# Optimization experiments

Hardware: AMD Instinct MI355X
Metric: run time of the kernel (lower is better)

## Reference

```python
import jax, jax.numpy as jnp
import numpy as np

N, E, IN = 50000, 800000, 128   # nodes, edges, input feature dim
H, C = 8, 32                    # heads, per-head channels
HC = H * C                      # 256 = concat width
NEG_SLOPE = 0.2
BN_EPS = 1e-5


def _gat_conv(x, src, dst, W, a_src, a_dst, b, heads, out_ch, concat):
    """PyG-style GATConv (eval mode, self-loops already in src/dst)."""
    n = x.shape[0]
    h = (x @ W).reshape(n, heads, out_ch)                 # [N,H,C]
    alpha_s = (h * a_src).sum(-1)                         # [N,H]
    alpha_d = (h * a_dst).sum(-1)                         # [N,H]
    e = jax.nn.leaky_relu(alpha_s[src] + alpha_d[dst], NEG_SLOPE)  # [Etot,H]
    # segment softmax over destination nodes (every node has a self-loop)
    emax = jax.ops.segment_max(e, dst, num_segments=n)    # [N,H]
    e = jnp.exp(e - emax[dst])
    denom = jax.ops.segment_sum(e, dst, num_segments=n)
    alpha = e / (denom[dst] + 1e-16)                      # [Etot,H]
    msg = h[src] * alpha[:, :, None]                      # [Etot,H,C]
    out = jax.ops.segment_sum(msg, dst, num_segments=n)   # [N,H,C]
    out = out.reshape(n, heads * out_ch) if concat else out.mean(axis=1)
    return out + b


def _bn(y, g, beta, m, v):
    return (y - m) * jax.lax.rsqrt(v + BN_EPS) * g + beta


def setup_inputs() -> dict:
    key = jax.random.key(0)
    ks = jax.random.split(key, 32)
    def p(i, shape, s=0.1):
        return jax.random.normal(ks[i], shape, dtype=jnp.float32) * s
    x = jax.random.normal(ks[0], (N, IN), dtype=jnp.float32)
    edge_index = jax.random.randint(ks[1], (2, E), 0, N, dtype=jnp.int32)
    d = dict(
        x=x, edge_index=edge_index,
        W1=p(2, (IN, HC)), a_src1=p(3, (H, C)), a_dst1=p(4, (H, C)), b1=p(5, (HC,)),
        bn1_g=jnp.ones((HC,), jnp.float32), bn1_b=jnp.zeros((HC,), jnp.float32),
        bn1_m=p(6, (HC,)), bn1_v=jax.random.uniform(ks[7], (HC,), jnp.float32, 0.5, 1.5),
        W2=p(8, (HC, HC)), a_src2=p(9, (H, C)), a_dst2=p(10, (H, C)), b2=p(11, (HC,)),
        bn2_g=jnp.ones((HC,), jnp.float32), bn2_b=jnp.zeros((HC,), jnp.float32),
        bn2_m=p(12, (HC,)), bn2_v=jax.random.uniform(ks[13], (HC,), jnp.float32, 0.5, 1.5),
        W3=p(14, (HC, C)), a_src3=p(15, (1, C)), a_dst3=p(16, (1, C)), b3=p(17, (C,)),
        Ws1=p(18, (IN, HC)), bs1=p(19, (HC,)),
        Ws2=p(20, (HC, C)), bs2=p(21, (C,)),
    )
    return d


def reference(x, edge_index, W1, a_src1, a_dst1, b1, bn1_g, bn1_b, bn1_m, bn1_v,
              W2, a_src2, a_dst2, b2, bn2_g, bn2_b, bn2_m, bn2_v,
              W3, a_src3, a_dst3, b3, Ws1, bs1, Ws2, bs2):
    n = x.shape[0]
    loops = jnp.arange(n, dtype=edge_index.dtype)
    src = jnp.concatenate([edge_index[0], loops])   # PyG add_self_loops=True
    dst = jnp.concatenate([edge_index[1], loops])
    x0 = x @ Ws1 + bs1                               # skip1
    h = _gat_conv(x, src, dst, W1, a_src1, a_dst1, b1, H, C, True)
    h = jax.nn.elu(_bn(h, bn1_g, bn1_b, bn1_m, bn1_v)) + x0
    xs = h @ Ws2 + bs2                               # skip2
    h2 = _gat_conv(h, src, dst, W2, a_src2, a_dst2, b2, H, C, True)
    h2 = jax.nn.elu(_bn(h2, bn2_g, bn2_b, bn2_m, bn2_v))
    out = _gat_conv(h2, src, dst, W3, a_src3, a_dst3, b3, 1, C, False) + xs
    return out
```

## Files before the change

### kernel.cpp

```cpp
#include <hip/hip_runtime.h>
#include <hip/hip_bf16.h>

#define NEG_SLOPE 0.2f
#define BN_EPS 1e-5f
#define BSH 8
#define STASH_CAP 6400

typedef __attribute__((ext_vector_type(8))) short bf16x8;
typedef __attribute__((ext_vector_type(4))) float f32x4;
typedef __attribute__((ext_vector_type(2))) float f32x2;

#if defined(__has_builtin)
#if __has_builtin(__builtin_amdgcn_cvt_f32_fp8) && __has_builtin(__builtin_amdgcn_cvt_pk_fp8_f32)
#define HW_FP8 1
#endif
#if __has_builtin(__builtin_amdgcn_cvt_pk_f32_fp8)
#define HW_FP8_PK 1
#endif
#endif

__device__ __forceinline__ float bf2f(unsigned short u) {
    union { unsigned int i; float f; } x;
    x.i = ((unsigned int)u) << 16;
    return x.f;
}
__device__ __forceinline__ unsigned short f2bf(float f) {
    __hip_bfloat16 b = __float2bfloat16(f);
    return *reinterpret_cast<unsigned short*>(&b);
}
__device__ __forceinline__ float lrelu(float v) {
    return v > 0.f ? v : NEG_SLOPE * v;
}
__device__ __forceinline__ void gload_lds16(const void* g, void* l) {
    __builtin_amdgcn_global_load_lds(
        (const __attribute__((address_space(1))) unsigned int*)(g),
        (__attribute__((address_space(3))) unsigned int*)(l),
        16, 0, 0);
}

__device__ __forceinline__ unsigned char f8enc(float f) {
#ifdef HW_FP8
    int p = __builtin_amdgcn_cvt_pk_fp8_f32(f, 0.f, 0, false);
    return (unsigned char)(p & 0xff);
#else
    float a = fabsf(f);
    unsigned int sign = (__float_as_uint(f) >> 31) << 7;
    if (a < 0.0009765625f) return (unsigned char)sign;
    a = fminf(a, 448.f);
    unsigned int bits = __float_as_uint(a);
    int e = (int)((bits >> 23) & 0xff) - 127;
    unsigned int mant = bits & 0x7fffff;
    if (e < -6) {
        int q = (int)(a * 512.f + 0.5f);
        if (q >= 8) return (unsigned char)(sign | 0x08);
        return (unsigned char)(sign | q);
    }
    unsigned int m = mant >> 20;
    unsigned int rem = mant & 0xfffff;
    if (rem > 0x80000 || (rem == 0x80000 && (m & 1))) m++;
    if (m == 8) { m = 0; e++; }
    if (e > 8) { e = 8; m = 6; }
    return (unsigned char)(sign | ((unsigned int)(e + 7) << 3) | m);
#endif
}
template <int SEL>
__device__ __forceinline__ float f8dec(unsigned int w) {
#ifdef HW_FP8
    return __builtin_amdgcn_cvt_f32_fp8(w, SEL);
#else
    unsigned int b = (w >> (SEL * 8)) & 0xff;
    unsigned int s = b >> 7, em = b & 0x7f;
    float mag;
    if (em >= 8) {
        unsigned int bits = (((em >> 3) + 120) << 23) | ((em & 7) << 20);
        mag = __uint_as_float(bits);
    } else {
        mag = (float)em * 0.001953125f;
    }
    return s ? -mag : mag;
#endif
}
__device__ __forceinline__ void fma_f8x4(float we, unsigned int wv, float4& acc) {
#ifdef HW_FP8_PK
    f32x2 lo = __builtin_amdgcn_cvt_pk_f32_fp8((int)wv, false);
    f32x2 hi = __builtin_amdgcn_cvt_pk_f32_fp8((int)wv, true);
    acc.x = fmaf(we, lo[0], acc.x);
    acc.y = fmaf(we, lo[1], acc.y);
    acc.z = fmaf(we, hi[0], acc.z);
    acc.w = fmaf(we, hi[1], acc.w);
#else
    acc.x = fmaf(we, f8dec<0>(wv), acc.x);
    acc.y = fmaf(we, f8dec<1>(wv), acc.y);
    acc.z = fmaf(we, f8dec<2>(wv), acc.z);
    acc.w = fmaf(we, f8dec<3>(wv), acc.w);
#endif
}

__device__ __forceinline__ int block_scan_incl(int v, int t) {
    int lane = t & 63, w = t >> 6;
    int sv = v;
    #pragma unroll
    for (int off = 1; off < 64; off <<= 1) {
        int u = __shfl_up(sv, off);
        if (lane >= off) sv += u;
    }
    __shared__ int ws_[4];
    if (lane == 63) ws_[w] = sv;
    __syncthreads();
    if (t == 0) {
        int a = 0;
        #pragma unroll
        for (int k = 0; k < 4; k++) { int x = ws_[k]; ws_[k] = a; a += x; }
    }
    __syncthreads();
    return sv + ws_[w];
}

__global__ __launch_bounds__(256) void phase1(const int* __restrict__ dstl,
                                              int E, int N, int NB,
                                              int* __restrict__ gHist,
                                              const float* __restrict__ x,
                                              unsigned short* __restrict__ xb, int n4x,
                                              const float* __restrict__ W1,
                                              const float* __restrict__ Ws1,
                                              const float* __restrict__ W2,
                                              const float* __restrict__ Ws2,
                                              const float* __restrict__ W3,
                                              const float* __restrict__ a_src1,
                                              const float* __restrict__ a_dst1,
                                              const float* __restrict__ a_src2,
                                              const float* __restrict__ a_dst2,
                                              const float* __restrict__ a_src3,
                                              const float* __restrict__ a_dst3,
                                              unsigned short* __restrict__ Wcat1,
                                              unsigned short* __restrict__ Wcat2,
                                              unsigned short* __restrict__ W3t) {
    int t = threadIdx.x;
    if (blockIdx.x < 256) {
        __shared__ int h[256];
        h[t] = 0;
        __syncthreads();
        int Etot = E + N;
        for (int i = blockIdx.x * 256 + t; i < Etot; i += 256 * 256) {
            int d = (i < E) ? dstl[i] : (i - E);
            atomicAdd(&h[d >> BSH], 1);
        }
        __syncthreads();
        if (t < NB && h[t]) atomicAdd(&gHist[t], h[t]);
        return;
    }
    int i = (blockIdx.x - 256) * 256 + t;
    if (i < n4x) {
        float4 v = reinterpret_cast<const float4*>(x)[i];
        ushort4 o;
        o.x = f2bf(v.x); o.y = f2bf(v.y); o.z = f2bf(v.z); o.w = f2bf(v.w);
        reinterpret_cast<ushort4*>(xb)[i] = o;
        return;
    }
    int j = i - n4x;
    if (j < 32768) {
        int m = j >> 7, k = j & 127;
        Wcat1[j] = f2bf(W1[k * 256 + m]);
    } else if (j < 65536) {
        int q = j - 32768; int m = q >> 7, k = q & 127;
        Wcat1[32768 + q] = f2bf(Ws1[k * 256 + m]);
    } else if (j < 131072) {
        int q = j - 65536; int m = q >> 8, k = q & 255;
        Wcat2[q] = f2bf(W2[k * 256 + m]);
    } else if (j < 139264) {
        int q = j - 131072; int m = q >> 8, k = q & 255;
        Wcat2[65536 + q] = f2bf(Ws2[k * 32 + m]);
    } else if (j < 147456) {
        int q = j - 139264; int m = q >> 8, k = q & 255;
        W3t[q] = f2bf(W3[k * 32 + m]);
    } else if (j < 149504) {
        int q = j - 147456; int r = q >> 7, k = q & 127;
        int h = r & 7;
        const float* av = (r < 8) ? a_src1 : a_dst1;
        float s = 0.f;
        #pragma unroll
        for (int c = 0; c < 32; c++) s += W1[k * 256 + h * 32 + c] * av[h * 32 + c];
        Wcat1[(512 + r) * 128 + k] = f2bf(s);
    } else if (j < 153600) {
        int q = j - 149504; int r = q >> 8, k = q & 255;
        int h = r & 7;
        const float* av = (r < 8) ? a_src2 : a_dst2;
        float s = 0.f;
        #pragma unroll
        for (int c = 0; c < 32; c++) s += W2[k * 256 + h * 32 + c] * av[h * 32 + c];
        Wcat2[(288 + r) * 256 + k] = f2bf(s);
    } else if (j < 154112) {
        int q = j - 153600; int r = q >> 8, k = q & 255;
        const float* av = r ? a_dst3 : a_src3;
        float s = 0.f;
        #pragma unroll
        for (int c = 0; c < 32; c++) s += W3[k * 32 + c] * av[c];
        W3t[(32 + r) * 256 + k] = f2bf(s);
    }
}

__global__ __launch_bounds__(256) void bucket_scatter(const int* __restrict__ srcl,
                                                      const int* __restrict__ dstl,
                                                      int E, int N, int NB,
                                                      const int* __restrict__ gHist,
                                                      int* __restrict__ gCursor,
                                                      unsigned int* __restrict__ bktEdges) {
    __shared__ unsigned int stage[4096];
    __shared__ int lbase[256];
    __shared__ int hist[256];
    __shared__ int bexcl[257];
    __shared__ int curk[256];
    __shared__ int gbase[256];
    int t = threadIdx.x;
    int Etot = E + N;
    int begin = blockIdx.x * 4096;

    int gv = (t < NB) ? gHist[t] : 0;
    int gincl = block_scan_incl(gv, t);
    lbase[t] = gincl - gv;
    __syncthreads();

    hist[t] = 0;
    __syncthreads();

    unsigned int ent[16];
    int eb[16];
    #pragma unroll
    for (int k = 0; k < 16; k++) {
        int i = begin + k * 256 + t;
        if (i < Etot) {
            int s, d;
            if (i < E) { s = srcl[i]; d = dstl[i]; }
            else       { s = d = i - E; }
            eb[k] = d >> BSH;
            ent[k] = ((unsigned int)s << BSH) | (unsigned int)(d & 255);
            atomicAdd(&hist[eb[k]], 1);
        } else eb[k] = -1;
    }
    __syncthreads();

    int v = hist[t];
    int incl = block_scan_incl(v, t);
    bexcl[t] = incl - v;
    curk[t] = incl - v;
    if (t == 255) bexcl[256] = incl;
    __syncthreads();

    #pragma unroll
    for (int k = 0; k < 16; k++) {
        if (eb[k] >= 0) {
            int slot = atomicAdd(&curk[eb[k]], 1);
            stage[slot] = ent[k];
        }
    }
    if (t < NB) {
        int cnt = hist[t];
        gbase[t] = cnt ? (lbase[t] + atomicAdd(&gCursor[t], cnt)) : 0;
    }
    __syncthreads();

    int total = bexcl[256];
    for (int p = t; p < total; p += 256) {
        int lo = 0, hi = NB - 1;
        while (lo < hi) {
            int mid = (lo + hi + 1) >> 1;
            if (bexcl[mid] <= p) lo = mid; else hi = mid - 1;
        }
        bktEdges[gbase[lo] + (p - bexcl[lo])] = stage[p];
    }
}

__global__ __launch_bounds__(256) void bucket_to_csr(const unsigned int* __restrict__ bktEdges,
                                                     const int* __restrict__ gHist,
                                                     int* __restrict__ indptr,
                                                     int* __restrict__ esrc,
                                                     int N, int NB, int Etot) {
    __shared__ int lbase[256];
    __shared__ int nh[256];
    __shared__ int ncur[256];
    __shared__ unsigned int stash[STASH_CAP];
    int b = blockIdx.x, t = threadIdx.x;

    int gv = (t < NB) ? gHist[t] : 0;
    int gincl = block_scan_incl(gv, t);
    lbase[t] = gincl - gv;
    __syncthreads();
    int base = lbase[b];
    int cnt = gHist[b];
    int nodeBase = b << BSH;

    nh[t] = 0;
    __syncthreads();
    for (int p = t; p < cnt; p += 256) {
        unsigned int e = bktEdges[base + p];
        if (p < STASH_CAP) stash[p] = e;
        atomicAdd(&nh[e & 255], 1);
    }
    __syncthreads();
    int v = nh[t];
    int incl = block_scan_incl(v, t);
    int excl = incl - v;
    ncur[t] = excl;
    if (nodeBase + t < N) indptr[nodeBase + t] = base + excl;
    __syncthreads();
    for (int p = t; p < cnt; p += 256) {
        unsigned int e = (p < STASH_CAP) ? stash[p] : bktEdges[base + p];
        int slot = atomicAdd(&ncur[e & 255], 1);
        esrc[base + slot] = (int)(e >> BSH);
    }
    if (b == 0 && t == 0) indptr[N] = Etot;
}

__global__ __launch_bounds__(256) void gemm_tile(const unsigned short* __restrict__ A,
                                                 const unsigned short* __restrict__ Bt,
                                                 unsigned short* __restrict__ outBf,
                                                 unsigned char* __restrict__ outQ,
                                                 unsigned short* __restrict__ outSk,
                                                 const float* __restrict__ biasSk,
                                                 float* __restrict__ asOut,
                                                 float* __restrict__ adOut,
                                                 int M, int K, int NCtot,
                                                 int split, int split2,
                                                 int ldBf, int ldSk) {
    __shared__ __align__(16) char smem[2][2][8192];
    int t = threadIdx.x;
    int w = t >> 6, lane = t & 63;
    int l16 = lane & 15, quad = lane >> 4;
    int warp_r = w >> 1, warp_c = w & 1;
    int rowBase = blockIdx.y * 128;
    int colBase = blockIdx.x * 128;

    int row_l = t & 127;
    int jchunk = t >> 7;
    int arow_st = rowBase + row_l; if (arow_st >= M) arow_st = M - 1;
    int bcol_st = colBase + row_l; if (bcol_st >= NCtot) bcol_st = NCtot - 1;
    const unsigned short* aRow = A + (size_t)arow_st * K;
    const unsigned short* bRow = Bt + (size_t)bcol_st * K;

    f32x4 acc[4][4];
    #pragma unroll
    for (int i = 0; i < 4; i++)
        #pragma unroll
        for (int j = 0; j < 4; j++) acc[i][j] = (f32x4){0.f, 0.f, 0.f, 0.f};

    auto stage = [&](int buf, int k0) {
        #pragma unroll
        for (int j = 0; j < 2; j++) {
            int chunk = j * 2 + jchunk;
            gload_lds16(aRow + k0 + chunk * 8, &smem[buf][0][(size_t)j * 4096 + (size_t)t * 16]);
            gload_lds16(bRow + k0 + chunk * 8, &smem[buf][1][(size_t)j * 4096 + (size_t)t * 16]);
        }
    };

    stage(0, 0);
    __syncthreads();
    int niter = K >> 5;
    for (int it = 0; it < niter; ++it) {
        if (it + 1 < niter) stage((it + 1) & 1, (it + 1) << 5);
        const char* Ab = &smem[it & 1][0][0];
        const char* Bb = &smem[it & 1][1][0];
        bf16x8 a[4], b[4];
        #pragma unroll
        for (int i = 0; i < 4; i++)
            a[i] = *reinterpret_cast<const bf16x8*>(Ab + quad * 2048 + (warp_r * 64 + i * 16 + l16) * 16);
        #pragma unroll
        for (int j = 0; j < 4; j++)
            b[j] = *reinterpret_cast<const bf16x8*>(Bb + quad * 2048 + (warp_c * 64 + j * 16 + l16) * 16);
        #pragma unroll
        for (int i = 0; i < 4; i++)
            #pragma unroll
            for (int j = 0; j < 4; j++)
                acc[i][j] = __builtin_amdgcn_mfma_f32_16x16x32_bf16(a[i], b[j], acc[i][j], 0, 0, 0);
        __syncthreads();
    }

    #pragma unroll
    for (int i = 0; i < 4; i++) {
        #pragma unroll
        for (int r = 0; r < 4; r++) {
            int row = rowBase + warp_r * 64 + i * 16 + quad * 4 + r;
            if (row >= M) continue;
            #pragma unroll
            for (int j = 0; j < 4; j++) {
                int c = colBase + warp_c * 64 + j * 16 + l16;
                if (c >= NCtot) continue;
                float v = acc[i][j][r];
                if (c < split) {
                    if (outBf) outBf[(size_t)row * ldBf + c] = f2bf(v);
                    if (outQ)  outQ[(size_t)row * ldBf + c] = f8enc(v);
                } else if (c < split2) {
                    outSk[(size_t)row * ldSk + (c - split)] = f2bf(v + biasSk[c - split]);
                } else {
                    int a = c - split2;
                    if (NCtot - split2 == 16) {
                        if (a < 8) asOut[(size_t)row * 8 + a] = v;
                        else       adOut[(size_t)row * 8 + a - 8] = v;
                    } else {
                        if (a == 0) asOut[row] = v;
                        else        adOut[row] = v;
                    }
                }
            }
        }
    }
}

template <int MODE>
__global__ __launch_bounds__(256) void agg256(const unsigned char* __restrict__ hq,
                                              const float* __restrict__ as,
                                              const float* __restrict__ ad,
                                              const int* __restrict__ indptr,
                                              const int* __restrict__ esrc,
                                              const float* __restrict__ bias,
                                              const float* __restrict__ bn_g,
                                              const float* __restrict__ bn_b,
                                              const float* __restrict__ bn_m,
                                              const float* __restrict__ bn_v,
                                              const unsigned short* __restrict__ skip,
                                              unsigned short* __restrict__ out, int N) {
    int t = threadIdx.x;
    int n = blockIdx.x * 4 + (t >> 6);
    if (n >= N) return;
    int lane = t & 63;
    int e8 = lane >> 3, h8 = lane & 7;
    int g4 = lane >> 4, cl = lane & 15;
    int hd = cl >> 1;
    int start = indptr[n], end = indptr[n + 1];
    int cnt = end - start;

    float adh = ad[n * 8 + h8];
    const unsigned char* hqc = hq + cl * 16;

    float4 acc0 = make_float4(0.f, 0.f, 0.f, 0.f);
    float4 acc1 = make_float4(0.f, 0.f, 0.f, 0.f);
    float4 acc2 = make_float4(0.f, 0.f, 0.f, 0.f);
    float4 acc3 = make_float4(0.f, 0.f, 0.f, 0.f);
    float sm = 0.f;
    int nfull = cnt & ~7;

    int sA = 0, sB = 0;
    float wA = 0.f, wB = 0.f;
    uint4 hv0 = {}, hv1 = {};
    if (nfull) {
        sA = esrc[start + e8];
        wA = __expf(lrelu(as[sA * 8 + h8] + adh));
        int r0 = __shfl(sA, g4 * 8);
        int r1 = __shfl(sA, (4 + g4) * 8);
        hv0 = *reinterpret_cast<const uint4*>(hqc + (size_t)r0 * 256);
        hv1 = *reinterpret_cast<const uint4*>(hqc + (size_t)r1 * 256);
        if (nfull > 8) {
            sB = esrc[start + 8 + e8];
            wB = __expf(lrelu(as[sB * 8 + h8] + adh));
        }
    }
    for (int i0 = start; i0 < start + nfull; i0 += 8) {
        uint4 u0 = hv0, u1 = hv1;
        float wcur = wA;
        if (i0 + 8 < start + nfull) {
            int r0 = __shfl(sB, g4 * 8);
            int r1 = __shfl(sB, (4 + g4) * 8);
            hv0 = *reinterpret_cast<const uint4*>(hqc + (size_t)r0 * 256);
            hv1 = *reinterpret_cast<const uint4*>(hqc + (size_t)r1 * 256);
        }
        sA = sB; wA = wB;
        if (i0 + 16 < start + nfull) {
            sB = esrc[i0 + 16 + e8];
            wB = __expf(lrelu(as[sB * 8 + h8] + adh));
        }
        sm += wcur;
        float w0 = __shfl(wcur, g4 * 8 + hd);
        float w1 = __shfl(wcur, (4 + g4) * 8 + hd);
        fma_f8x4(w0, u0.x, acc0);
        fma_f8x4(w0, u0.y, acc1);
        fma_f8x4(w0, u0.z, acc2);
        fma_f8x4(w0, u0.w, acc3);
        fma_f8x4(w1, u1.x, acc0);
        fma_f8x4(w1, u1.y, acc1);
        fma_f8x4(w1, u1.z, acc2);
        fma_f8x4(w1, u1.w, acc3);
    }
    int rem = cnt - nfull;
    if (rem) {
        int i0 = start + nfull;
        int idx = i0 + e8;
        bool valid = idx < end;
        int s_r = esrc[valid ? idx : end - 1];
        float w_r = valid ? __expf(lrelu(as[s_r * 8 + h8] + adh)) : 0.f;
        sm += w_r;
        int r0 = __shfl(s_r, g4 * 8);
        uint4 u0 = *reinterpret_cast<const uint4*>(hqc + (size_t)r0 * 256);
        float w0 = __shfl(w_r, g4 * 8 + hd);
        fma_f8x4(w0, u0.x, acc0);
        fma_f8x4(w0, u0.y, acc1);
        fma_f8x4(w0, u0.z, acc2);
        fma_f8x4(w0, u0.w, acc3);
        if (rem > 4) {
            int r1 = __shfl(s_r, (4 + g4) * 8);
            uint4 u1 = *reinterpret_cast<const uint4*>(hqc + (size_t)r1 * 256);
            float w1 = __shfl(w_r, (4 + g4) * 8 + hd);
            fma_f8x4(w1, u1.x, acc0);
            fma_f8x4(w1, u1.y, acc1);
            fma_f8x4(w1, u1.z, acc2);
            fma_f8x4(w1, u1.w, acc3);
        }
    }

    acc0.x += __shfl_xor(acc0.x, 16); acc0.y += __shfl_xor(acc0.y, 16);
    acc0.z += __shfl_xor(acc0.z, 16); acc0.w += __shfl_xor(acc0.w, 16);
    acc0.x += __shfl_xor(acc0.x, 32); acc0.y += __shfl_xor(acc0.y, 32);
    acc0.z += __shfl_xor(acc0.z, 32); acc0.w += __shfl_xor(acc0.w, 32);
    acc1.x += __shfl_xor(acc1.x, 16); acc1.y += __shfl_xor(acc1.y, 16);
    acc1.z += __shfl_xor(acc1.z, 16); acc1.w += __shfl_xor(acc1.w, 16);
    acc1.x += __shfl_xor(acc1.x, 32); acc1.y += __shfl_xor(acc1.y, 32);
    acc1.z += __shfl_xor(acc1.z, 32); acc1.w += __shfl_xor(acc1.w, 32);
    acc2.x += __shfl_xor(acc2.x, 16); acc2.y += __shfl_xor(acc2.y, 16);
    acc2.z += __shfl_xor(acc2.z, 16); acc2.w += __shfl_xor(acc2.w, 16);
    acc2.x += __shfl_xor(acc2.x, 32); acc2.y += __shfl_xor(acc2.y, 32);
    acc2.z += __shfl_xor(acc2.z, 32); acc2.w += __shfl_xor(acc2.w, 32);
    acc3.x += __shfl_xor(acc3.x, 16); acc3.y += __shfl_xor(acc3.y, 16);
    acc3.z += __shfl_xor(acc3.z, 16); acc3.w += __shfl_xor(acc3.w, 16);
    acc3.x += __shfl_xor(acc3.x, 32); acc3.y += __shfl_xor(acc3.y, 32);
    acc3.z += __shfl_xor(acc3.z, 32); acc3.w += __shfl_xor(acc3.w, 32);

    #pragma unroll
    for (int off = 8; off < 64; off <<= 1) sm += __shfl_xor(sm, off);
    float il = 1.f / (sm + 1e-16f);
    float il_c = __shfl(il, hd);

    float4 my;
    if (g4 == 0)      my = acc0;
    else if (g4 == 1) my = acc1;
    else if (g4 == 2) my = acc2;
    else              my = acc3;
    int cb = cl * 16 + g4 * 4;

    float4 bv  = *reinterpret_cast<const float4*>(&bias[cb]);
    float4 gv  = *reinterpret_cast<const float4*>(&bn_g[cb]);
    float4 bbv = *reinterpret_cast<const float4*>(&bn_b[cb]);
    float4 mv  = *reinterpret_cast<const float4*>(&bn_m[cb]);
    float4 vv  = *reinterpret_cast<const float4*>(&bn_v[cb]);
    float o[4] = {my.x * il_c + bv.x, my.y * il_c + bv.y,
                  my.z * il_c + bv.z, my.w * il_c + bv.w};
    float g[4] = {gv.x, gv.y, gv.z, gv.w}, bb[4] = {bbv.x, bbv.y, bbv.z, bbv.w};
    float m[4] = {mv.x, mv.y, mv.z, mv.w}, vr[4] = {vv.x, vv.y, vv.z, vv.w};
    float sk[4] = {0.f, 0.f, 0.f, 0.f};
    if (MODE == 1) {
        ushort4 s4 = *reinterpret_cast<const ushort4*>(&skip[(size_t)n * 256 + cb]);
        sk[0] = bf2f(s4.x); sk[1] = bf2f(s4.y); sk[2] = bf2f(s4.z); sk[3] = bf2f(s4.w);
    }
    ushort4 res;
    unsigned short* rp = &res.x;
    #pragma unroll
    for (int j = 0; j < 4; j++) {
        float val = (o[j] - m[j]) * rsqrtf(vr[j] + BN_EPS) * g[j] + bb[j];
        val = val > 0.f ? val : (__expf(val) - 1.f);
        val += sk[j];
        rp[j] = f2bf(val);
    }
    *reinterpret_cast<ushort4*>(&out[(size_t)n * 256 + cb]) = res;
}

__global__ __launch_bounds__(256) void agg32(const unsigned short* __restrict__ h3,
                                             const float* __restrict__ as,
                                             const float* __restrict__ ad,
                                             const int* __restrict__ indptr,
                                             const int* __restrict__ esrc,
                                             const float* __restrict__ b3,
                                             const unsigned short* __restrict__ xs,
                                             float* __restrict__ out, int N) {
    int t = threadIdx.x;
    int n = blockIdx.x * 4 + (t >> 6);
    if (n >= N) return;
    int lane = t & 63;
    int e_sub = lane >> 3, c4 = (lane & 7) * 4;
    int start = indptr[n], end = indptr[n + 1];
    float adn = ad[n];

    float4 acc = make_float4(0.f, 0.f, 0.f, 0.f);
    float sm = 0.f;
    int i0 = start;
    for (; i0 + 16 <= end; i0 += 16) {
        int sA = esrc[i0 + e_sub];
        int sB = esrc[i0 + 8 + e_sub];
        float wA = __expf(lrelu(as[sA] + adn));
        float wB = __expf(lrelu(as[sB] + adn));
        sm += wA + wB;
        ushort4 hA = *reinterpret_cast<const ushort4*>(&h3[(size_t)sA * 32 + c4]);
        ushort4 hB = *reinterpret_cast<const ushort4*>(&h3[(size_t)sB * 32 + c4]);
        acc.x = fmaf(wA, bf2f(hA.x), acc.x); acc.y = fmaf(wA, bf2f(hA.y), acc.y);
        acc.z = fmaf(wA, bf2f(hA.z), acc.z); acc.w = fmaf(wA, bf2f(hA.w), acc.w);
        acc.x = fmaf(wB, bf2f(hB.x), acc.x); acc.y = fmaf(wB, bf2f(hB.y), acc.y);
        acc.z = fmaf(wB, bf2f(hB.z), acc.z); acc.w = fmaf(wB, bf2f(hB.w), acc.w);
    }
    for (; i0 < end; i0 += 8) {
        int idx = i0 + e_sub;
        bool valid = idx < end;
        if (valid) {
            int s = esrc[idx];
            float w = __expf(lrelu(as[s] + adn));
            sm += w;
            ushort4 hv = *reinterpret_cast<const ushort4*>(&h3[(size_t)s * 32 + c4]);
            acc.x = fmaf(w, bf2f(hv.x), acc.x);
            acc.y = fmaf(w, bf2f(hv.y), acc.y);
            acc.z = fmaf(w, bf2f(hv.z), acc.z);
            acc.w = fmaf(w, bf2f(hv.w), acc.w);
        }
    }
    #pragma unroll
    for (int off = 8; off < 64; off <<= 1) {
        sm    += __shfl_xor(sm, off);
        acc.x += __shfl_xor(acc.x, off);
        acc.y += __shfl_xor(acc.y, off);
        acc.z += __shfl_xor(acc.z, off);
        acc.w += __shfl_xor(acc.w, off);
    }
    if (e_sub == 0) {
        float il = 1.f / (sm + 1e-16f);
        float4 bv = *reinterpret_cast<const float4*>(&b3[c4]);
        ushort4 xv = *reinterpret_cast<const ushort4*>(&xs[(size_t)n * 32 + c4]);
        float4 o;
        o.x = acc.x * il + bv.x + bf2f(xv.x);
        o.y = acc.y * il + bv.y + bf2f(xv.y);
        o.z = acc.z * il + bv.z + bf2f(xv.z);
        o.w = acc.w * il + bv.w + bf2f(xv.w);
        *reinterpret_cast<float4*>(&out[(size_t)n * 32 + c4]) = o;
    }
}

extern "C" void kernel_launch(void* const* d_in, const int* in_sizes, int n_in,
                              void* d_out, int out_size, void* d_ws, size_t ws_size,
                              hipStream_t stream) {
    const float* x      = (const float*)d_in[0];
    const int*   eidx   = (const int*)  d_in[1];
    const float* W1     = (const float*)d_in[2];
    const float* a_src1 = (const float*)d_in[3];
    const float* a_dst1 = (const float*)d_in[4];
    const float* b1     = (const float*)d_in[5];
    const float* bn1_g  = (const float*)d_in[6];
    const float* bn1_b  = (const float*)d_in[7];
    const float* bn1_m  = (const float*)d_in[8];
    const float* bn1_v  = (const float*)d_in[9];
    const float* W2     = (const float*)d_in[10];
    const float* a_src2 = (const float*)d_in[11];
    const float* a_dst2 = (const float*)d_in[12];
    const float* b2     = (const float*)d_in[13];
    const float* bn2_g  = (const float*)d_in[14];
    const float* bn2_b  = (const float*)d_in[15];
    const float* bn2_m  = (const float*)d_in[16];
    const float* bn2_v  = (const float*)d_in[17];
    const float* W3     = (const float*)d_in[18];
    const float* a_src3 = (const float*)d_in[19];
    const float* a_dst3 = (const float*)d_in[20];
    const float* b3     = (const float*)d_in[21];
    const float* Ws1    = (const float*)d_in[22];
    const float* bs1    = (const float*)d_in[23];
    const float* Ws2    = (const float*)d_in[24];
    const float* bs2    = (const float*)d_in[25];

    const int N = in_sizes[0] / 128;
    const int E = in_sizes[1] / 2;
    const int Etot = E + N;
    const int NB = (N + 255) >> 8;
    const int* srcl = eidx;
    const int* dstl = eidx + E;

    char* ws = (char*)d_ws;
    size_t off = 0;
    auto alloc = [&](size_t bytes) -> void* {
        void* p = ws + off;
        off += (bytes + 255) & ~(size_t)255;
        return p;
    };
    unsigned short* xb    = (unsigned short*)alloc((size_t)N * 128 * 2);
    unsigned short* feat  = (unsigned short*)alloc((size_t)N * 256 * 2);
    unsigned char*  hq    = (unsigned char*)alloc((size_t)N * 256);
    unsigned short* h2b   = (unsigned short*)alloc((size_t)N * 256 * 2);
    unsigned short* featb = (unsigned short*)alloc((size_t)N * 256 * 2);
    unsigned short* xsbuf = (unsigned short*)alloc((size_t)N * 32 * 2);
    unsigned short* h3b   = (unsigned short*)alloc((size_t)N * 32 * 2);
    float*          asb   = (float*)alloc((size_t)N * 8 * 4);
    float*          adb   = (float*)alloc((size_t)N * 8 * 4);
    unsigned short* Wcat1 = (unsigned short*)alloc((size_t)528 * 128 * 2);
    unsigned short* Wcat2 = (unsigned short*)alloc((size_t)304 * 256 * 2);
    unsigned short* W3t   = (unsigned short*)alloc((size_t)34 * 256 * 2);
    int* gHC     = (int*)alloc(512 * 4);
    int* gHist   = gHC;
    int* gCursor = gHC + 256;
    unsigned int* bktEdges = (unsigned int*)alloc((size_t)Etot * 4);
    int* indptr  = (int*)alloc((size_t)(N + 1) * 4);
    int* esrc    = (int*)alloc((size_t)Etot * 4);
    (void)ws_size; (void)n_in; (void)out_size;

    hipMemsetAsync(gHC, 0, 512 * 4, stream);
    int n4x = N * 128 / 4;
    int prepBlocks = (n4x + 154112 + 255) / 256;
    phase1<<<256 + prepBlocks, 256, 0, stream>>>(dstl, E, N, NB, gHist,
                                                 x, xb, n4x,
                                                 W1, Ws1, W2, Ws2, W3,
                                                 a_src1, a_dst1, a_src2, a_dst2,
                                                 a_src3, a_dst3,
                                                 Wcat1, Wcat2, W3t);
    bucket_scatter<<<(Etot + 4095) / 4096, 256, 0, stream>>>(srcl, dstl, E, N, NB,
                                                             gHist, gCursor, bktEdges);
    bucket_to_csr<<<NB, 256, 0, stream>>>(bktEdges, gHist, indptr, esrc, N, NB, Etot);

    int gy128 = (N + 127) / 128;
    int gn4 = (N + 3) / 4;

    gemm_tile<<<dim3(5, gy128), 256, 0, stream>>>(xb, Wcat1, nullptr, hq, feat, bs1,
                                                  asb, adb,
                                                  N, 128, 528, 256, 512, 256, 256);
    agg256<1><<<gn4, 256, 0, stream>>>(hq, asb, adb, indptr, esrc, b1,
                                       bn1_g, bn1_b, bn1_m, bn1_v, feat, h2b, N);

    gemm_tile<<<dim3(3, gy128), 256, 0, stream>>>(h2b, Wcat2, nullptr, hq, xsbuf, bs2,
                                                  asb, adb,
                                                  N, 256, 304, 256, 288, 256, 32);
    agg256<0><<<gn4, 256, 0, stream>>>(hq, asb, adb, indptr, esrc, b2,
                                       bn2_g, bn2_b, bn2_m, bn2_v, nullptr, featb, N);

    gemm_tile<<<dim3(1, gy128), 256, 0, stream>>>(featb, W3t, h3b, nullptr, nullptr, nullptr,
                                                  asb, adb,
                                                  N, 256, 34, 32, 32, 32, 32);
    agg32<<<gn4, 256, 0, stream>>>(h3b, asb, adb, indptr, esrc, b3, xsbuf,
                                   (float*)d_out, N);
}
```

Before: 383.9 us.

## Load GEMM MFMA operands directly from global memory instead of LDS staging

Removes the double-buffered LDS staging (global_load_lds plus barriers) in the tiled GEMM. Each lane now loads its bf16x8 A/B fragments straight from global memory every k-step. This drops the shared memory use and the per-iteration __syncthreads, so more blocks can be resident. The cost is that data is no longer shared across warps within a tile, so global/L2 traffic rises and load latency is no longer hidden by prefetching.

```diff
diff --git a/kernel.cpp b/kernel.cpp
--- a/kernel.cpp
+++ b/kernel.cpp
@@ -30,12 +30,6 @@
 }
 __device__ __forceinline__ float lrelu(float v) {
     return v > 0.f ? v : NEG_SLOPE * v;
-}
-__device__ __forceinline__ void gload_lds16(const void* g, void* l) {
-    __builtin_amdgcn_global_load_lds(
-        (const __attribute__((address_space(1))) unsigned int*)(g),
-        (__attribute__((address_space(3))) unsigned int*)(l),
-        16, 0, 0);
 }
 
 __device__ __forceinline__ unsigned char f8enc(float f) {
@@ -322,7 +316,6 @@
                                                  int M, int K, int NCtot,
                                                  int split, int split2,
                                                  int ldBf, int ldSk) {
-    __shared__ __align__(16) char smem[2][2][8192];
     int t = threadIdx.x;
     int w = t >> 6, lane = t & 63;
     int l16 = lane & 15, quad = lane >> 4;
@@ -330,12 +323,28 @@
     int rowBase = blockIdx.y * 128;
     int colBase = blockIdx.x * 128;
 
-    int row_l = t & 127;
-    int jchunk = t >> 7;
-    int arow_st = rowBase + row_l; if (arow_st >= M) arow_st = M - 1;
-    int bcol_st = colBase + row_l; if (bcol_st >= NCtot) bcol_st = NCtot - 1;
-    const unsigned short* aRow = A + (size_t)arow_st * K;
-    const unsigned short* bRow = Bt + (size_t)bcol_st * K;
+    const unsigned short* aP0; const unsigned short* aP1;
+    const unsigned short* aP2; const unsigned short* aP3;
+    const unsigned short* bP0; const unsigned short* bP1;
+    const unsigned short* bP2; const unsigned short* bP3;
+    {
+        int r0 = rowBase + warp_r * 64 + 0 * 16 + l16; if (r0 >= M) r0 = M - 1;
+        int r1 = rowBase + warp_r * 64 + 1 * 16 + l16; if (r1 >= M) r1 = M - 1;
+        int r2 = rowBase + warp_r * 64 + 2 * 16 + l16; if (r2 >= M) r2 = M - 1;
+        int r3 = rowBase + warp_r * 64 + 3 * 16 + l16; if (r3 >= M) r3 = M - 1;
+        aP0 = A + (size_t)r0 * K + quad * 8;
+        aP1 = A + (size_t)r1 * K + quad * 8;
+        aP2 = A + (size_t)r2 * K + quad * 8;
+        aP3 = A + (size_t)r3 * K + quad * 8;
+        int c0 = colBase + warp_c * 64 + 0 * 16 + l16; if (c0 >= NCtot) c0 = NCtot - 1;
+        int c1 = colBase + warp_c * 64 + 1 * 16 + l16; if (c1 >= NCtot) c1 = NCtot - 1;
+        int c2 = colBase + warp_c * 64 + 2 * 16 + l16; if (c2 >= NCtot) c2 = NCtot - 1;
+        int c3 = colBase + warp_c * 64 + 3 * 16 + l16; if (c3 >= NCtot) c3 = NCtot - 1;
+        bP0 = Bt + (size_t)c0 * K + quad * 8;
+        bP1 = Bt + (size_t)c1 * K + quad * 8;
+        bP2 = Bt + (size_t)c2 * K + quad * 8;
+        bP3 = Bt + (size_t)c3 * K + quad * 8;
+    }
 
     f32x4 acc[4][4];
     #pragma unroll
@@ -343,35 +352,23 @@
         #pragma unroll
         for (int j = 0; j < 4; j++) acc[i][j] = (f32x4){0.f, 0.f, 0.f, 0.f};
 
-    auto stage = [&](int buf, int k0) {
-        #pragma unroll
-        for (int j = 0; j < 2; j++) {
-            int chunk = j * 2 + jchunk;
-            gload_lds16(aRow + k0 + chunk * 8, &smem[buf][0][(size_t)j * 4096 + (size_t)t * 16]);
-            gload_lds16(bRow + k0 + chunk * 8, &smem[buf][1][(size_t)j * 4096 + (size_t)t * 16]);
-        }
-    };
-
-    stage(0, 0);
-    __syncthreads();
     int niter = K >> 5;
     for (int it = 0; it < niter; ++it) {
-        if (it + 1 < niter) stage((it + 1) & 1, (it + 1) << 5);
-        const char* Ab = &smem[it & 1][0][0];
-        const char* Bb = &smem[it & 1][1][0];
+        int k0 = it << 5;
         bf16x8 a[4], b[4];
-        #pragma unroll
-        for (int i = 0; i < 4; i++)
-            a[i] = *reinterpret_cast<const bf16x8*>(Ab + quad * 2048 + (warp_r * 64 + i * 16 + l16) * 16);
-        #pragma unroll
-        for (int j = 0; j < 4; j++)
-            b[j] = *reinterpret_cast<const bf16x8*>(Bb + quad * 2048 + (warp_c * 64 + j * 16 + l16) * 16);
+        a[0] = *reinterpret_cast<const bf16x8*>(aP0 + k0);
+        a[1] = *reinterpret_cast<const bf16x8*>(aP1 + k0);
+        a[2] = *reinterpret_cast<const bf16x8*>(aP2 + k0);
+        a[3] = *reinterpret_cast<const bf16x8*>(aP3 + k0);
+        b[0] = *reinterpret_cast<const bf16x8*>(bP0 + k0);
+        b[1] = *reinterpret_cast<const bf16x8*>(bP1 + k0);
+        b[2] = *reinterpret_cast<const bf16x8*>(bP2 + k0);
+        b[3] = *reinterpret_cast<const bf16x8*>(bP3 + k0);
         #pragma unroll
         for (int i = 0; i < 4; i++)
             #pragma unroll
             for (int j = 0; j < 4; j++)
                 acc[i][j] = __builtin_amdgcn_mfma_f32_16x16x32_bf16(a[i], b[j], acc[i][j], 0, 0, 0);
-        __syncthreads();
     }
 
     #pragma unroll
```

Result: slower. 401.9 us (+4.7%).
